# Kernel tuning notes

Measured on AMD Instinct MI355X. Metric: run time of the kernel, lower is better.

## Reference

```python
import jax, jax.numpy as jnp
import numpy as np

NUM_PITCHES = 88
H_FEAT = 188
LSTM_UNITS = 48
N_STATES = 5
CTX_HID = 16
CTX_OUT = 4


def _glorot(key, shape):
    fan_in, fan_out = shape[1], shape[0]
    lim = (6.0 / (fan_in + fan_out)) ** 0.5
    return jax.random.uniform(key, shape, jnp.float32, -lim, lim)


def setup_inputs() -> dict:
    key = jax.random.key(0)
    ks = jax.random.split(key, 16)
    B, T = 16, 256
    pitch_features = jax.random.normal(ks[0], (B, NUM_PITCHES, H_FEAT, T), jnp.float32)
    prev_context = jax.random.uniform(ks[1], (B, NUM_PITCHES, 3), jnp.float32)
    # context net params
    fc1_w = _glorot(ks[2], (CTX_HID, 3)); fc1_b = jnp.zeros((CTX_HID,), jnp.float32)
    fc2_w = _glorot(ks[3], (CTX_HID, CTX_HID)); fc2_b = jnp.zeros((CTX_HID,), jnp.float32)
    fc3_w = _glorot(ks[4], (CTX_OUT, CTX_HID)); fc3_b = jnp.zeros((CTX_OUT,), jnp.float32)
    # lstm1: input H_FEAT+4 -> 48; gates order i,f,g,o (torch convention)
    in1 = H_FEAT + CTX_OUT
    lstm1_wih = _glorot(ks[5], (4 * LSTM_UNITS, in1))
    lstm1_whh = _glorot(ks[6], (4 * LSTM_UNITS, LSTM_UNITS))
    lstm1_bih = jnp.zeros((4 * LSTM_UNITS,), jnp.float32)
    lstm1_bhh = jnp.zeros((4 * LSTM_UNITS,), jnp.float32)
    lstm2_wih = _glorot(ks[7], (4 * LSTM_UNITS, LSTM_UNITS))
    lstm2_whh = _glorot(ks[8], (4 * LSTM_UNITS, LSTM_UNITS))
    lstm2_bih = jnp.zeros((4 * LSTM_UNITS,), jnp.float32)
    lstm2_bhh = jnp.zeros((4 * LSTM_UNITS,), jnp.float32)
    fc_states_w = _glorot(ks[9], (N_STATES, LSTM_UNITS))
    fc_states_b = jnp.zeros((N_STATES,), jnp.float32)
    return dict(pitch_features=pitch_features, prev_context=prev_context,
                fc1_w=fc1_w, fc1_b=fc1_b, fc2_w=fc2_w, fc2_b=fc2_b,
                fc3_w=fc3_w, fc3_b=fc3_b,
                lstm1_wih=lstm1_wih, lstm1_whh=lstm1_whh, lstm1_bih=lstm1_bih, lstm1_bhh=lstm1_bhh,
                lstm2_wih=lstm2_wih, lstm2_whh=lstm2_whh, lstm2_bih=lstm2_bih, lstm2_bhh=lstm2_bhh,
                fc_states_w=fc_states_w, fc_states_b=fc_states_b)


def _lstm_scan(x, wih, whh, bih, bhh):
    # x: (S, N, In); zero init state; returns (S, N, U)
    S, N, _ = x.shape
    U = whh.shape[1]
    xg = jnp.einsum('sni,gi->sng', x, wih) + bih + bhh  # precompute input gates

    def step(carry, xg_t):
        h, c = carry
        g = xg_t + h @ whh.T  # (N, 4U)
        i, f, gg, o = jnp.split(g, 4, axis=-1)
        c = jax.nn.sigmoid(f) * c + jax.nn.sigmoid(i) * jnp.tanh(gg)
        h = jax.nn.sigmoid(o) * jnp.tanh(c)
        return (h, c), h

    init = (jnp.zeros((N, U), x.dtype), jnp.zeros((N, U), x.dtype))
    _, hs = jax.lax.scan(step, init, xg)
    return hs


def reference(pitch_features, prev_context,
              fc1_w, fc1_b, fc2_w, fc2_b, fc3_w, fc3_b,
              lstm1_wih, lstm1_whh, lstm1_bih, lstm1_bhh,
              lstm2_wih, lstm2_whh, lstm2_bih, lstm2_bhh,
              fc_states_w, fc_states_b):
    B, P, H, T = pitch_features.shape
    # Context net (context never updates across t in the original loop)
    x = jax.nn.relu(prev_context @ fc1_w.T + fc1_b)
    x = jax.nn.relu(x @ fc2_w.T + fc2_b)
    ctx_emb = x @ fc3_w.T + fc3_b  # (B, P, 4)
    # Each timestep t is independent: LSTM runs over the pitch axis (len 88)
    # with zero initial state every step. Fold (B, T) into batch N.
    pf = jnp.transpose(pitch_features, (1, 0, 3, 2)).reshape(P, B * T, H)  # (P, BT, H)
    ce = jnp.broadcast_to(ctx_emb[:, None, :, :], (B, T, P, CTX_OUT))
    ce = jnp.transpose(ce, (2, 0, 1, 3)).reshape(P, B * T, CTX_OUT)
    seq = jnp.concatenate([pf, ce], axis=-1)  # (P, BT, H+4)
    h = _lstm_scan(seq, lstm1_wih, lstm1_whh, lstm1_bih, lstm1_bhh)
    h = _lstm_scan(h, lstm2_wih, lstm2_whh, lstm2_bih, lstm2_bhh)
    logits = h @ fc_states_w.T + fc_states_b  # (P, BT, 5)
    logits = logits.reshape(P, B, T, N_STATES)
    logits = jnp.transpose(logits, (1, 0, 3, 2))  # (B, P, 5, T)
    return jax.nn.softmax(logits, axis=2)
```

## Files before the change

kernel.cpp:

```cpp
#include <hip/hip_runtime.h>
#include <hip/hip_bf16.h>
#include <cstdint>

#define P_ 88
#define B_ 16
#define T_ 256
#define H_ 188
#define G_ 192
#define U_ 48
#define N_ 4096

typedef __attribute__((ext_vector_type(8))) short bf16x8;
typedef __attribute__((ext_vector_type(8))) _Float16 f16x8;
typedef __attribute__((ext_vector_type(4))) float f32x4;

__device__ __forceinline__ float sigf(float x) {
  return __builtin_amdgcn_rcpf(1.0f + __expf(-x));
}
__device__ __forceinline__ float tanh_f(float x) {
  return 1.0f - 2.0f * __builtin_amdgcn_rcpf(1.0f + __expf(2.0f * x));
}
__device__ __forceinline__ float hs2f(unsigned short s) {
  union { unsigned short u; _Float16 h; } x;
  x.u = s;
  return (float)x.h;
}
__device__ __forceinline__ unsigned short f2hs(float v) {
  union { _Float16 h; unsigned short s; } x;
  x.h = (_Float16)v;
  return x.s;
}

__device__ __forceinline__ void lds_barrier() {
  asm volatile("s_waitcnt lgkmcnt(0)\n\ts_barrier" ::: "memory");
}

__global__ void ctx_kernel(const float* __restrict__ pc,
                           const float* __restrict__ fc1w, const float* __restrict__ fc1b,
                           const float* __restrict__ fc2w, const float* __restrict__ fc2b,
                           const float* __restrict__ fc3w, const float* __restrict__ fc3b,
                           const float* __restrict__ wih1,
                           const float* __restrict__ bih1, const float* __restrict__ bhh1,
                           float* __restrict__ ctxg) {
  int bp = blockIdx.x * 64 + threadIdx.x;
  if (bp >= B_ * P_) return;
  float p0 = pc[bp * 3 + 0], p1 = pc[bp * 3 + 1], p2 = pc[bp * 3 + 2];
  float x1[16], x2[16];
#pragma unroll
  for (int jj = 0; jj < 16; ++jj)
    x1[jj] = fmaxf(0.f, fc1w[jj * 3 + 0] * p0 + fc1w[jj * 3 + 1] * p1 + fc1w[jj * 3 + 2] * p2 + fc1b[jj]);
#pragma unroll
  for (int jj = 0; jj < 16; ++jj) {
    float s = fc2b[jj];
#pragma unroll
    for (int i = 0; i < 16; ++i) s += fc2w[jj * 16 + i] * x1[i];
    x2[jj] = fmaxf(0.f, s);
  }
  float ce[4];
#pragma unroll
  for (int jj = 0; jj < 4; ++jj) {
    float s = fc3b[jj];
#pragma unroll
    for (int i = 0; i < 16; ++i) s += fc3w[jj * 16 + i] * x2[i];
    ce[jj] = s;
  }
  float* op = ctxg + (size_t)bp * G_;
  for (int g = 0; g < G_; ++g) {
    const float* wr = wih1 + (size_t)g * G_ + H_;
    op[g] = bih1[g] + bhh1[g] + ce[0] * wr[0] + ce[1] * wr[1] + ce[2] * wr[2] + ce[3] * wr[3];
  }
}

__global__ __launch_bounds__(256) void wfrag_kernel(const float* __restrict__ wih1,
                                                    f16x8* __restrict__ wfrag) {
  const int idx = blockIdx.x * 256 + threadIdx.x;
  if (idx >= 12 * 6 * 64) return;
  const int l = idx & 63;
  const int kc = (idx >> 6) % 6;
  const int j = idx / 384;
  const int g = j * 16 + (l & 15);
  const int k0 = kc * 32 + (l >> 4) * 8;
  f16x8 v;
#pragma unroll
  for (int e = 0; e < 8; ++e) {
    const int k = k0 + e;
    const float wv = (k < H_) ? wih1[(size_t)g * G_ + k] : 0.f;
    v[e] = (_Float16)wv;
  }
  wfrag[idx] = v;
}

__global__ __launch_bounds__(256, 3) void gemm_mfma(const float* __restrict__ pf,
                                                    const f16x8* __restrict__ wfrag,
                                                    const float* __restrict__ ctxg,
                                                    unsigned short* __restrict__ xg2) {
  const int bp = blockIdx.x >> 1, tb = blockIdx.x & 1;
  const int p = bp % P_, b = bp / P_;
  const int tid = threadIdx.x;
  const int w = tid >> 6, l = tid & 63;
  const int lj = l & 15, lq = l >> 4;

  __shared__ __align__(16) char ldsraw[49152];
  _Float16(*Ahi)[34] = (_Float16(*)[34])ldsraw;
  _Float16(*Alo)[34] = (_Float16(*)[34])(ldsraw + 8704);

  float cg[12];
#pragma unroll
  for (int jn = 0; jn < 12; ++jn)
    cg[jn] = ctxg[(size_t)bp * G_ + jn * 16 + lj];

  f32x4 acc[2][12];
#pragma unroll
  for (int mt = 0; mt < 2; ++mt)
#pragma unroll
    for (int jn = 0; jn < 12; ++jn)
#pragma unroll
      for (int r = 0; r < 4; ++r) acc[mt][jn][r] = 0.f;

  const float* Ab = pf + (size_t)bp * H_ * T_ + tb * 128;
  const int kl = tid >> 5;
  const int t4 = (tid & 31) * 4;

  for (int kc = 0; kc < 6; ++kc) {
    __syncthreads();
#pragma unroll
    for (int rr = 0; rr < 4; ++rr) {
      const int kk = rr * 8 + kl;
      const int kg = kc * 32 + kk;
      float a0 = 0.f, a1 = 0.f, a2 = 0.f, a3 = 0.f;
      if (kg < H_) {
        const float4 v = *(const float4*)(Ab + (size_t)kg * T_ + t4);
        a0 = v.x; a1 = v.y; a2 = v.z; a3 = v.w;
      }
      const _Float16 h0 = (_Float16)a0, h1 = (_Float16)a1;
      const _Float16 h2 = (_Float16)a2, h3 = (_Float16)a3;
      Ahi[t4 + 0][kk] = h0; Alo[t4 + 0][kk] = (_Float16)(a0 - (float)h0);
      Ahi[t4 + 1][kk] = h1; Alo[t4 + 1][kk] = (_Float16)(a1 - (float)h1);
      Ahi[t4 + 2][kk] = h2; Alo[t4 + 2][kk] = (_Float16)(a2 - (float)h2);
      Ahi[t4 + 3][kk] = h3; Alo[t4 + 3][kk] = (_Float16)(a3 - (float)h3);
    }
    __syncthreads();
    const int trow = w * 32;
    const f16x8 ahi0 = *(const f16x8*)&Ahi[trow + lj][lq * 8];
    const f16x8 ahi1 = *(const f16x8*)&Ahi[trow + 16 + lj][lq * 8];
    const f16x8 alo0 = *(const f16x8*)&Alo[trow + lj][lq * 8];
    const f16x8 alo1 = *(const f16x8*)&Alo[trow + 16 + lj][lq * 8];
#pragma unroll
    for (int jn = 0; jn < 12; ++jn) {
      const f16x8 wf = wfrag[(jn * 6 + kc) * 64 + l];
      acc[0][jn] = __builtin_amdgcn_mfma_f32_16x16x32_f16(ahi0, wf, acc[0][jn], 0, 0, 0);
      acc[1][jn] = __builtin_amdgcn_mfma_f32_16x16x32_f16(ahi1, wf, acc[1][jn], 0, 0, 0);
      acc[0][jn] = __builtin_amdgcn_mfma_f32_16x16x32_f16(alo0, wf, acc[0][jn], 0, 0, 0);
      acc[1][jn] = __builtin_amdgcn_mfma_f32_16x16x32_f16(alo1, wf, acc[1][jn], 0, 0, 0);
    }
  }
  __syncthreads();

  unsigned short* Cst = (unsigned short*)ldsraw + w * 6144;
#pragma unroll
  for (int mt = 0; mt < 2; ++mt)
#pragma unroll
    for (int jn = 0; jn < 12; ++jn)
#pragma unroll
      for (int r = 0; r < 4; ++r)
        Cst[mt * 3072 + jn * 256 + r * 64 + l] = f2hs(acc[mt][jn][r] + cg[jn]);
  const int nb0 = b * 16 + tb * 8 + w * 2;
  unsigned short* gb = xg2 + ((size_t)p * 256 + nb0) * 3072;
#pragma unroll
  for (int rr = 0; rr < 12; ++rr) {
    const uint4 v = *(const uint4*)(Cst + rr * 512 + l * 8);
    *(uint4*)(gb + rr * 512 + l * 8) = v;
  }
}

__global__ __launch_bounds__(256, 2) void scan_mfma(
    const unsigned short* __restrict__ xg2,
    const float* __restrict__ whh1, const float* __restrict__ wih2,
    const float* __restrict__ whh2, const float* __restrict__ bih2,
    const float* __restrict__ bhh2, const float* __restrict__ fcw,
    const float* __restrict__ fcb, float* __restrict__ out) {
  __shared__ __align__(16) _Float16 h12[16][104];
  __shared__ __align__(16) float gs1[8][196];
  __shared__ __align__(16) float gs2[8][196];
  __shared__ __align__(16) float h2f[8][52];
  __shared__ __align__(16) float fcws[5 * 48];
  __shared__ float logit_s[5][8];
  __shared__ float prob_s[5][8];

  const int tid = threadIdx.x;
  const int w = tid >> 6;
  const int l = tid & 63;
  const int lj = l & 15;
  const int lq = l >> 4;
  const int grp = blockIdx.x >> 1;
  const int half = blockIdx.x & 1;
  const int n0 = blockIdx.x * 8;
  const int b = n0 >> 8, t0 = n0 & 255;

  f16x8 b1[3][2];
  f16x8 b2f[3][3];
  float bias2r[3];
#pragma unroll
  for (int i = 0; i < 3; ++i) {
    const int j = w * 48 + i * 16 + lj;
    bias2r[i] = bih2[j] + bhh2[j];
#pragma unroll
    for (int kc = 0; kc < 2; ++kc)
#pragma unroll
      for (int e = 0; e < 8; ++e) {
        const int u = kc * 32 + lq * 8 + e;
        b1[i][kc][e] = (u < U_) ? (_Float16)whh1[j * U_ + u] : (_Float16)0.f;
      }
#pragma unroll
    for (int kc = 0; kc < 3; ++kc)
#pragma unroll
      for (int e = 0; e < 8; ++e) {
        const int k = kc * 32 + lq * 8 + e;
        b2f[i][kc][e] = (k < U_) ? (_Float16)wih2[j * U_ + k]
                                 : (_Float16)whh2[j * U_ + (k - U_)];
      }
  }

  for (int e = tid; e < 16 * 104 / 2; e += 256) ((unsigned int*)h12)[e] = 0u;
  for (int e = tid; e < 5 * U_; e += 256) fcws[e] = fcw[e];

  const int tn0 = tid / U_, tu0 = tid % U_;
  const int tn1 = (256 + tid) / U_, tu1 = (256 + tid) % U_;
  const bool has2 = (tid < 128);
  float c1s[2] = {0.f, 0.f}, c2s[2] = {0.f, 0.f};

  const bool fcth = tid < 40;
  const int fk = tid >> 3, fn = tid & 7;
  const float fcbr = fcth ? fcb[fk] : 0.f;
  const bool stth = tid >= 96 && tid < 136;
  const int sk = (tid - 96) >> 3, sn = (tid - 96) & 7;
  const bool smth = tid >= 192 && tid < 200;
  const int smn = tid - 192;

  unsigned short xp[12];
  {
    const size_t pb = (size_t)grp * 3072;
#pragma unroll
    for (int i = 0; i < 3; ++i)
#pragma unroll
      for (int r = 0; r < 4; ++r)
        xp[i * 4 + r] = (lq < 2)
            ? xg2[pb + (size_t)((w * 3 + i) * 256 + r * 64 + (half * 2 + lq) * 16 + lj)]
            : (unsigned short)0;
  }
  lds_barrier();

  for (int p = -1; p < P_; ++p) {
    const _Float16* hr = &h12[lj][0];
    const f16x8 f0 = *(const f16x8*)(hr + lq * 8);
    const f16x8 f1 = *(const f16x8*)(hr + 32 + lq * 8);
    const f16x8 f2 = *(const f16x8*)(hr + 64 + lq * 8);
    if (p >= 0) {
      f32x4 dH[3];
#pragma unroll
      for (int i = 0; i < 3; ++i) {
        dH[i][0] = bias2r[i]; dH[i][1] = bias2r[i];
        dH[i][2] = bias2r[i]; dH[i][3] = bias2r[i];
      }
#pragma unroll
      for (int i = 0; i < 3; ++i)
        dH[i] = __builtin_amdgcn_mfma_f32_16x16x32_f16(f0, b2f[i][0], dH[i], 0, 0, 0);
#pragma unroll
      for (int i = 0; i < 3; ++i)
        dH[i] = __builtin_amdgcn_mfma_f32_16x16x32_f16(f1, b2f[i][1], dH[i], 0, 0, 0);
#pragma unroll
      for (int i = 0; i < 3; ++i)
        dH[i] = __builtin_amdgcn_mfma_f32_16x16x32_f16(f2, b2f[i][2], dH[i], 0, 0, 0);
      if (lq < 2) {
#pragma unroll
        for (int i = 0; i < 3; ++i)
#pragma unroll
          for (int r = 0; r < 4; ++r)
            gs2[lq * 4 + r][w * 48 + i * 16 + lj] = dH[i][r];
      }
    }
    if (p >= 1 && fcth) {
      float a = fcbr;
#pragma unroll
      for (int uq = 0; uq < 12; ++uq) {
        f32x4 hv = *(const f32x4*)&h2f[fn][uq * 4];
        f32x4 wv = *(const f32x4*)&fcws[fk * 48 + uq * 4];
        a += hv[0] * wv[0] + hv[1] * wv[1] + hv[2] * wv[2] + hv[3] * wv[3];
      }
      logit_s[fk][fn] = a;
    }
    if (p >= 2 && stth) {
      out[(((size_t)b * P_ + (p - 2)) * 5 + sk) * T_ + t0 + sn] = prob_s[sk][sn];
    }
    __builtin_amdgcn_sched_barrier(0);
    if (p < P_ - 1) {
      f32x4 cH[3];
#pragma unroll
      for (int i = 0; i < 3; ++i)
#pragma unroll
        for (int r = 0; r < 4; ++r) cH[i][r] = hs2f(xp[i * 4 + r]);
      if (p < P_ - 2) {
        const size_t pb = (size_t)((p + 2) * 256 + grp) * 3072;
#pragma unroll
        for (int i = 0; i < 3; ++i)
#pragma unroll
          for (int r = 0; r < 4; ++r)
            xp[i * 4 + r] = (lq < 2)
                ? xg2[pb + (size_t)((w * 3 + i) * 256 + r * 64 + (half * 2 + lq) * 16 + lj)]
                : (unsigned short)0;
      }
#pragma unroll
      for (int i = 0; i < 3; ++i)
        cH[i] = __builtin_amdgcn_mfma_f32_16x16x32_f16(f0, b1[i][0], cH[i], 0, 0, 0);
#pragma unroll
      for (int i = 0; i < 3; ++i)
        cH[i] = __builtin_amdgcn_mfma_f32_16x16x32_f16(f1, b1[i][1], cH[i], 0, 0, 0);
      if (lq < 2) {
#pragma unroll
        for (int i = 0; i < 3; ++i)
#pragma unroll
          for (int r = 0; r < 4; ++r)
            gs1[lq * 4 + r][w * 48 + i * 16 + lj] = cH[i][r];
      }
    }
    lds_barrier();
    if (p >= 0) {
      {
        const int n = tn0, u = tu0;
        const float ig = gs2[n][u], fg = gs2[n][48 + u];
        const float gg = gs2[n][96 + u], og = gs2[n][144 + u];
        const float cc = sigf(fg) * c2s[0] + sigf(ig) * tanh_f(gg);
        c2s[0] = cc;
        const float h = sigf(og) * tanh_f(cc);
        h12[n][48 + u] = (_Float16)h;
        h2f[n][u] = h;
      }
      if (has2) {
        const int n = tn1, u = tu1;
        const float ig = gs2[n][u], fg = gs2[n][48 + u];
        const float gg = gs2[n][96 + u], og = gs2[n][144 + u];
        const float cc = sigf(fg) * c2s[1] + sigf(ig) * tanh_f(gg);
        c2s[1] = cc;
        const float h = sigf(og) * tanh_f(cc);
        h12[n][48 + u] = (_Float16)h;
        h2f[n][u] = h;
      }
    }
    if (p < P_ - 1) {
      {
        const int n = tn0, u = tu0;
        const float ig = gs1[n][u], fg = gs1[n][48 + u];
        const float gg = gs1[n][96 + u], og = gs1[n][144 + u];
        const float cc = sigf(fg) * c1s[0] + sigf(ig) * tanh_f(gg);
        c1s[0] = cc;
        h12[n][u] = (_Float16)(sigf(og) * tanh_f(cc));
      }
      if (has2) {
        const int n = tn1, u = tu1;
        const float ig = gs1[n][u], fg = gs1[n][48 + u];
        const float gg = gs1[n][96 + u], og = gs1[n][144 + u];
        const float cc = sigf(fg) * c1s[1] + sigf(ig) * tanh_f(gg);
        c1s[1] = cc;
        h12[n][u] = (_Float16)(sigf(og) * tanh_f(cc));
      }
    }
    if (p >= 1 && smth) {
      const int n = smn;
      const float l0 = logit_s[0][n], l1 = logit_s[1][n], l2 = logit_s[2][n],
                  l3 = logit_s[3][n], l4 = logit_s[4][n];
      const float m = fmaxf(fmaxf(fmaxf(l0, l1), fmaxf(l2, l3)), l4);
      const float e0 = __expf(l0 - m), e1 = __expf(l1 - m), e2 = __expf(l2 - m),
                  e3 = __expf(l3 - m), e4 = __expf(l4 - m);
      const float rs = __builtin_amdgcn_rcpf(e0 + e1 + e2 + e3 + e4);
      prob_s[0][n] = e0 * rs; prob_s[1][n] = e1 * rs; prob_s[2][n] = e2 * rs;
      prob_s[3][n] = e3 * rs; prob_s[4][n] = e4 * rs;
    }
    lds_barrier();
  }
  if (fcth) {
    float a = fcbr;
#pragma unroll
    for (int uq = 0; uq < 12; ++uq) {
      f32x4 hv = *(const f32x4*)&h2f[fn][uq * 4];
      f32x4 wv = *(const f32x4*)&fcws[fk * 48 + uq * 4];
      a += hv[0] * wv[0] + hv[1] * wv[1] + hv[2] * wv[2] + hv[3] * wv[3];
    }
    logit_s[fk][fn] = a;
  }
  if (stth) {
    out[(((size_t)b * P_ + (P_ - 2)) * 5 + sk) * T_ + t0 + sn] = prob_s[sk][sn];
  }
  lds_barrier();
  if (smth) {
    const int n = smn;
    const float l0 = logit_s[0][n], l1 = logit_s[1][n], l2 = logit_s[2][n],
                l3 = logit_s[3][n], l4 = logit_s[4][n];
    const float m = fmaxf(fmaxf(fmaxf(l0, l1), fmaxf(l2, l3)), l4);
    const float e0 = __expf(l0 - m), e1 = __expf(l1 - m), e2 = __expf(l2 - m),
                e3 = __expf(l3 - m), e4 = __expf(l4 - m);
    const float rs = __builtin_amdgcn_rcpf(e0 + e1 + e2 + e3 + e4);
    prob_s[0][n] = e0 * rs; prob_s[1][n] = e1 * rs; prob_s[2][n] = e2 * rs;
    prob_s[3][n] = e3 * rs; prob_s[4][n] = e4 * rs;
  }
  lds_barrier();
  if (stth) {
    out[(((size_t)b * P_ + (P_ - 1)) * 5 + sk) * T_ + t0 + sn] = prob_s[sk][sn];
  }
}

extern "C" void kernel_launch(void* const* d_in, const int* in_sizes, int n_in,
                              void* d_out, int out_size, void* d_ws, size_t ws_size,
                              hipStream_t stream) {
  const float* pf   = (const float*)d_in[0];
  const float* pc   = (const float*)d_in[1];
  const float* fc1w = (const float*)d_in[2];
  const float* fc1b = (const float*)d_in[3];
  const float* fc2w = (const float*)d_in[4];
  const float* fc2b = (const float*)d_in[5];
  const float* fc3w = (const float*)d_in[6];
  const float* fc3b = (const float*)d_in[7];
  const float* wih1 = (const float*)d_in[8];
  const float* whh1 = (const float*)d_in[9];
  const float* bih1 = (const float*)d_in[10];
  const float* bhh1 = (const float*)d_in[11];
  const float* wih2 = (const float*)d_in[12];
  const float* whh2 = (const float*)d_in[13];
  const float* bih2 = (const float*)d_in[14];
  const float* bhh2 = (const float*)d_in[15];
  const float* fcw  = (const float*)d_in[16];
  const float* fcb  = (const float*)d_in[17];
  float* out = (float*)d_out;

  char* wsp = (char*)d_ws;
  float* ctxg = (float*)wsp;
  const size_t CTXG_BYTES = (size_t)B_ * P_ * G_ * sizeof(float);
  f16x8* wfrag = (f16x8*)(wsp + CTXG_BYTES);
  const size_t WFRAG_BYTES = (size_t)12 * 6 * 64 * 16;
  unsigned short* xg2 = (unsigned short*)(wsp + CTXG_BYTES + WFRAG_BYTES);

  ctx_kernel<<<22, 64, 0, stream>>>(pc, fc1w, fc1b, fc2w, fc2b, fc3w, fc3b,
                                    wih1, bih1, bhh1, ctxg);
  wfrag_kernel<<<18, 256, 0, stream>>>(wih1, wfrag);
  gemm_mfma<<<B_ * P_ * 2, 256, 0, stream>>>(pf, wfrag, ctxg, xg2);
  scan_mfma<<<N_ / 8, 256, 0, stream>>>(xg2, whh1, wih2, whh2,
                                        bih2, bhh2, fcw, fcb, out);
}
```

Before: 397.2 us.

## Permute gate columns so LSTM cell update runs in MFMA registers via lane shuffles

Reorders the gate columns of the layer-1 input projection and of the layer-2 weights so each 16-column MFMA tile holds all four gates for a set of units. The cell update can then be done directly on the MFMA accumulators using xor-lane shuffles, instead of scattering gates to shared memory and reading them back after a barrier. The hidden-state buffer becomes double-buffered, which lets the layer-2 and layer-1 steps each finish within their own phase. The FC, store and softmax work is spread across waves. The goal is to cut LDS round trips and per-step barrier work on the serial recurrence, at the cost of shuffle overhead and more complex index mapping.

```diff
diff --git a/kernel.cpp b/kernel.cpp
--- a/kernel.cpp
+++ b/kernel.cpp
@@ -33,6 +33,28 @@
 
 __device__ __forceinline__ void lds_barrier() {
   asm volatile("s_waitcnt lgkmcnt(0)\n\ts_barrier" ::: "memory");
+}
+
+__device__ __forceinline__ void qtrans(const f32x4 v, int l,
+                                       float& g0, float& g1, float& g2, float& g3) {
+  const bool qo = (l & 1);
+  const float e0 = __shfl_xor((float)v[1], 1);
+  const float e1 = __shfl_xor((float)v[0], 1);
+  const float e2 = __shfl_xor((float)v[3], 1);
+  const float e3 = __shfl_xor((float)v[2], 1);
+  const float a0 = qo ? e0 : v[0];
+  const float a1 = qo ? v[1] : e1;
+  const float a2 = qo ? e2 : v[2];
+  const float a3 = qo ? v[3] : e3;
+  const bool q2 = (l & 2);
+  const float f0 = __shfl_xor(a2, 2);
+  const float f1 = __shfl_xor(a3, 2);
+  const float f2 = __shfl_xor(a0, 2);
+  const float f3 = __shfl_xor(a1, 2);
+  g0 = q2 ? f0 : a0;
+  g1 = q2 ? f1 : a1;
+  g2 = q2 ? a2 : f2;
+  g3 = q2 ? a3 : f3;
 }
 
 __global__ void ctx_kernel(const float* __restrict__ pc,
@@ -160,10 +182,18 @@
 #pragma unroll
   for (int mt = 0; mt < 2; ++mt)
 #pragma unroll
-    for (int jn = 0; jn < 12; ++jn)
+    for (int jn = 0; jn < 12; ++jn) {
+      const int g = jn * 16 + lj;
+      const int t = g / 48;
+      const int rem = g - 48 * t;
+      const int sw = rem / 12;
+      const int ul = rem - 12 * sw;
+      const int c = ul * 4 + t;
+      const int slot = (sw * 3 + (c >> 4)) * 256 + lq * 16 + (c & 15);
 #pragma unroll
       for (int r = 0; r < 4; ++r)
-        Cst[mt * 3072 + jn * 256 + r * 64 + l] = f2hs(acc[mt][jn][r] + cg[jn]);
+        Cst[mt * 3072 + slot + r * 64] = f2hs(acc[mt][jn][r] + cg[jn]);
+    }
   const int nb0 = b * 16 + tb * 8 + w * 2;
   unsigned short* gb = xg2 + ((size_t)p * 256 + nb0) * 3072;
 #pragma unroll
@@ -179,21 +209,16 @@
     const float* __restrict__ whh2, const float* __restrict__ bih2,
     const float* __restrict__ bhh2, const float* __restrict__ fcw,
     const float* __restrict__ fcb, float* __restrict__ out) {
-  __shared__ __align__(16) _Float16 h12[16][104];
-  __shared__ __align__(16) float gs1[8][196];
-  __shared__ __align__(16) float gs2[8][196];
-  __shared__ __align__(16) float h2f[8][52];
+  __shared__ __align__(16) _Float16 hbuf[2][16][120];
+  __shared__ __align__(16) float h2f[2][8][52];
   __shared__ __align__(16) float fcws[5 * 48];
   __shared__ float logit_s[5][8];
   __shared__ float prob_s[5][8];
 
   const int tid = threadIdx.x;
-  const int w = tid >> 6;
-  const int l = tid & 63;
-  const int lj = l & 15;
-  const int lq = l >> 4;
-  const int grp = blockIdx.x >> 1;
-  const int half = blockIdx.x & 1;
+  const int w = tid >> 6, l = tid & 63;
+  const int lj = l & 15, lq = l >> 4;
+  const int grp = blockIdx.x >> 1, half = blockIdx.x & 1;
   const int n0 = blockIdx.x * 8;
   const int b = n0 >> 8, t0 = n0 & 255;
 
@@ -202,7 +227,9 @@
   float bias2r[3];
 #pragma unroll
   for (int i = 0; i < 3; ++i) {
-    const int j = w * 48 + i * 16 + lj;
+    const int c = i * 16 + lj;
+    const int ul = c >> 2, t = c & 3;
+    const int j = t * 48 + w * 12 + ul;
     bias2r[i] = bih2[j] + bhh2[j];
 #pragma unroll
     for (int kc = 0; kc < 2; ++kc)
@@ -221,21 +248,23 @@
       }
   }
 
-  for (int e = tid; e < 16 * 104 / 2; e += 256) ((unsigned int*)h12)[e] = 0u;
+  for (int e = tid; e < 2 * 16 * 120 / 2; e += 256) ((unsigned int*)hbuf)[e] = 0u;
+  for (int e = tid; e < 2 * 8 * 52; e += 256) ((float*)h2f)[e] = 0.f;
   for (int e = tid; e < 5 * U_; e += 256) fcws[e] = fcw[e];
 
-  const int tn0 = tid / U_, tu0 = tid % U_;
-  const int tn1 = (256 + tid) / U_, tu1 = (256 + tid) % U_;
-  const bool has2 = (tid < 128);
-  float c1s[2] = {0.f, 0.f}, c2s[2] = {0.f, 0.f};
-
-  const bool fcth = tid < 40;
-  const int fk = tid >> 3, fn = tid & 7;
+  const int qn = lq * 4 + (l & 3);
+  const int kk = (l >> 2) & 3;
+  float c1s[3] = {0.f, 0.f, 0.f}, c2s[3] = {0.f, 0.f, 0.f};
+
+  const bool fcth = (l >= 32 && l < 42);
+  const int fi = w * 10 + (l - 32);
+  const int fk = (fi >> 3) < 5 ? (fi >> 3) : 0, fn = fi & 7;
   const float fcbr = fcth ? fcb[fk] : 0.f;
-  const bool stth = tid >= 96 && tid < 136;
-  const int sk = (tid - 96) >> 3, sn = (tid - 96) & 7;
-  const bool smth = tid >= 192 && tid < 200;
-  const int smn = tid - 192;
+  const bool stth = (l >= 42 && l < 52);
+  const int ts = w * 10 + (l - 42);
+  const int sk = (ts >> 3) < 5 ? (ts >> 3) : 0, sn = ts & 7;
+  const bool smth = (l >= 52 && l < 54);
+  const int smn = w * 2 + (l - 52);
 
   unsigned short xp[12];
   {
@@ -251,11 +280,13 @@
   lds_barrier();
 
   for (int p = -1; p < P_; ++p) {
-    const _Float16* hr = &h12[lj][0];
-    const f16x8 f0 = *(const f16x8*)(hr + lq * 8);
-    const f16x8 f1 = *(const f16x8*)(hr + 32 + lq * 8);
-    const f16x8 f2 = *(const f16x8*)(hr + 64 + lq * 8);
+    const int cur = p & 1, alt = cur ^ 1;
     if (p >= 0) {
+      const _Float16* hc = &hbuf[cur][lj][0];
+      const _Float16* ha = &hbuf[alt][lj][0];
+      const f16x8 f0 = *(const f16x8*)(hc + lq * 8);
+      const f16x8 f1 = *(const f16x8*)(((lq < 2) ? hc : ha) + 32 + lq * 8);
+      const f16x8 f2 = *(const f16x8*)(ha + 64 + lq * 8);
       f32x4 dH[3];
 #pragma unroll
       for (int i = 0; i < 3; ++i) {
@@ -271,29 +302,36 @@
 #pragma unroll
       for (int i = 0; i < 3; ++i)
         dH[i] = __builtin_amdgcn_mfma_f32_16x16x32_f16(f2, b2f[i][2], dH[i], 0, 0, 0);
-      if (lq < 2) {
-#pragma unroll
-        for (int i = 0; i < 3; ++i)
-#pragma unroll
-          for (int r = 0; r < 4; ++r)
-            gs2[lq * 4 + r][w * 48 + i * 16 + lj] = dH[i][r];
-      }
-    }
-    if (p >= 1 && fcth) {
-      float a = fcbr;
-#pragma unroll
-      for (int uq = 0; uq < 12; ++uq) {
-        f32x4 hv = *(const f32x4*)&h2f[fn][uq * 4];
-        f32x4 wv = *(const f32x4*)&fcws[fk * 48 + uq * 4];
-        a += hv[0] * wv[0] + hv[1] * wv[1] + hv[2] * wv[2] + hv[3] * wv[3];
-      }
-      logit_s[fk][fn] = a;
-    }
-    if (p >= 2 && stth) {
-      out[(((size_t)b * P_ + (p - 2)) * 5 + sk) * T_ + t0 + sn] = prob_s[sk][sn];
-    }
-    __builtin_amdgcn_sched_barrier(0);
+      if (l < 32) {
+#pragma unroll
+        for (int i = 0; i < 3; ++i) {
+          float g0, g1, g2, g3;
+          qtrans(dH[i], l, g0, g1, g2, g3);
+          const float cc = sigf(g1) * c2s[i] + sigf(g0) * tanh_f(g2);
+          c2s[i] = cc;
+          const float h = sigf(g3) * tanh_f(cc);
+          const int u = w * 12 + i * 4 + kk;
+          hbuf[cur][qn][48 + u] = (_Float16)h;
+          h2f[cur][qn][u] = h;
+        }
+      } else if (fcth && p >= 1) {
+        float a = fcbr;
+#pragma unroll
+        for (int uq = 0; uq < 12; ++uq) {
+          f32x4 hv = *(const f32x4*)&h2f[alt][fn][uq * 4];
+          f32x4 wv = *(const f32x4*)&fcws[fk * 48 + uq * 4];
+          a += hv[0] * wv[0] + hv[1] * wv[1] + hv[2] * wv[2] + hv[3] * wv[3];
+        }
+        logit_s[fk][fn] = a;
+      } else if (stth && p >= 2) {
+        out[(((size_t)b * P_ + (p - 2)) * 5 + sk) * T_ + t0 + sn] = prob_s[sk][sn];
+      }
+    }
+    lds_barrier();
     if (p < P_ - 1) {
+      const _Float16* hc = &hbuf[cur][lj][0];
+      const f16x8 f0 = *(const f16x8*)(hc + lq * 8);
+      const f16x8 f1 = *(const f16x8*)(hc + 32 + lq * 8);
       f32x4 cH[3];
 #pragma unroll
       for (int i = 0; i < 3; ++i)
@@ -315,56 +353,19 @@
 #pragma unroll
       for (int i = 0; i < 3; ++i)
         cH[i] = __builtin_amdgcn_mfma_f32_16x16x32_f16(f1, b1[i][1], cH[i], 0, 0, 0);
-      if (lq < 2) {
-#pragma unroll
-        for (int i = 0; i < 3; ++i)
-#pragma unroll
-          for (int r = 0; r < 4; ++r)
-            gs1[lq * 4 + r][w * 48 + i * 16 + lj] = cH[i][r];
-      }
-    }
-    lds_barrier();
-    if (p >= 0) {
-      {
-        const int n = tn0, u = tu0;
-        const float ig = gs2[n][u], fg = gs2[n][48 + u];
-        const float gg = gs2[n][96 + u], og = gs2[n][144 + u];
-        const float cc = sigf(fg) * c2s[0] + sigf(ig) * tanh_f(gg);
-        c2s[0] = cc;
-        const float h = sigf(og) * tanh_f(cc);
-        h12[n][48 + u] = (_Float16)h;
-        h2f[n][u] = h;
-      }
-      if (has2) {
-        const int n = tn1, u = tu1;
-        const float ig = gs2[n][u], fg = gs2[n][48 + u];
-        const float gg = gs2[n][96 + u], og = gs2[n][144 + u];
-        const float cc = sigf(fg) * c2s[1] + sigf(ig) * tanh_f(gg);
-        c2s[1] = cc;
-        const float h = sigf(og) * tanh_f(cc);
-        h12[n][48 + u] = (_Float16)h;
-        h2f[n][u] = h;
-      }
-    }
-    if (p < P_ - 1) {
-      {
-        const int n = tn0, u = tu0;
-        const float ig = gs1[n][u], fg = gs1[n][48 + u];
-        const float gg = gs1[n][96 + u], og = gs1[n][144 + u];
-        const float cc = sigf(fg) * c1s[0] + sigf(ig) * tanh_f(gg);
-        c1s[0] = cc;
-        h12[n][u] = (_Float16)(sigf(og) * tanh_f(cc));
-      }
-      if (has2) {
-        const int n = tn1, u = tu1;
-        const float ig = gs1[n][u], fg = gs1[n][48 + u];
-        const float gg = gs1[n][96 + u], og = gs1[n][144 + u];
-        const float cc = sigf(fg) * c1s[1] + sigf(ig) * tanh_f(gg);
-        c1s[1] = cc;
-        h12[n][u] = (_Float16)(sigf(og) * tanh_f(cc));
-      }
-    }
-    if (p >= 1 && smth) {
+      if (l < 32) {
+#pragma unroll
+        for (int i = 0; i < 3; ++i) {
+          float g0, g1, g2, g3;
+          qtrans(cH[i], l, g0, g1, g2, g3);
+          const float cc = sigf(g1) * c1s[i] + sigf(g0) * tanh_f(g2);
+          c1s[i] = cc;
+          const int u = w * 12 + i * 4 + kk;
+          hbuf[alt][qn][u] = (_Float16)(sigf(g3) * tanh_f(cc));
+        }
+      }
+    }
+    if (smth && p >= 1) {
       const int n = smn;
       const float l0 = logit_s[0][n], l1 = logit_s[1][n], l2 = logit_s[2][n],
                   l3 = logit_s[3][n], l4 = logit_s[4][n];
@@ -377,11 +378,12 @@
     }
     lds_barrier();
   }
+  const int parL = (P_ - 1) & 1;
   if (fcth) {
     float a = fcbr;
 #pragma unroll
     for (int uq = 0; uq < 12; ++uq) {
-      f32x4 hv = *(const f32x4*)&h2f[fn][uq * 4];
+      f32x4 hv = *(const f32x4*)&h2f[parL][fn][uq * 4];
       f32x4 wv = *(const f32x4*)&fcws[fk * 48 + uq * 4];
       a += hv[0] * wv[0] + hv[1] * wv[1] + hv[2] * wv[2] + hv[3] * wv[3];
     }
```

After: 487.7 us. +22.8%, slower.

## Fuse LSTM1 input-projection GEMM into the recurrent scan kernel with double-buffered staging

Applied to the files above, without the earlier changes.

Removes the separate wfrag and gemm_mfma kernels and the fp16 xg2 intermediate buffer. The scan kernel now holds W_ih1 fragments in registers and computes each pitch's input gates itself with MFMA on hi/lo split fp16 features. The features for the next pitch are prefetched into double-buffered LDS while the current step runs. This avoids writing and re-reading the large gate tensor through global memory. In exchange the serial scan loop gets 36 extra MFMAs per step plus heavier register pressure, which may lower occupancy.

```diff
diff --git a/kernel.cpp b/kernel.cpp
--- a/kernel.cpp
+++ b/kernel.cpp
@@ -10,7 +10,6 @@
 #define U_ 48
 #define N_ 4096
 
-typedef __attribute__((ext_vector_type(8))) short bf16x8;
 typedef __attribute__((ext_vector_type(8))) _Float16 f16x8;
 typedef __attribute__((ext_vector_type(4))) float f32x4;
 
@@ -19,16 +18,6 @@
 }
 __device__ __forceinline__ float tanh_f(float x) {
   return 1.0f - 2.0f * __builtin_amdgcn_rcpf(1.0f + __expf(2.0f * x));
-}
-__device__ __forceinline__ float hs2f(unsigned short s) {
-  union { unsigned short u; _Float16 h; } x;
-  x.u = s;
-  return (float)x.h;
-}
-__device__ __forceinline__ unsigned short f2hs(float v) {
-  union { _Float16 h; unsigned short s; } x;
-  x.h = (_Float16)v;
-  return x.s;
 }
 
 __device__ __forceinline__ void lds_barrier() {
@@ -71,114 +60,13 @@
   }
 }
 
-__global__ __launch_bounds__(256) void wfrag_kernel(const float* __restrict__ wih1,
-                                                    f16x8* __restrict__ wfrag) {
-  const int idx = blockIdx.x * 256 + threadIdx.x;
-  if (idx >= 12 * 6 * 64) return;
-  const int l = idx & 63;
-  const int kc = (idx >> 6) % 6;
-  const int j = idx / 384;
-  const int g = j * 16 + (l & 15);
-  const int k0 = kc * 32 + (l >> 4) * 8;
-  f16x8 v;
-#pragma unroll
-  for (int e = 0; e < 8; ++e) {
-    const int k = k0 + e;
-    const float wv = (k < H_) ? wih1[(size_t)g * G_ + k] : 0.f;
-    v[e] = (_Float16)wv;
-  }
-  wfrag[idx] = v;
-}
-
-__global__ __launch_bounds__(256, 3) void gemm_mfma(const float* __restrict__ pf,
-                                                    const f16x8* __restrict__ wfrag,
-                                                    const float* __restrict__ ctxg,
-                                                    unsigned short* __restrict__ xg2) {
-  const int bp = blockIdx.x >> 1, tb = blockIdx.x & 1;
-  const int p = bp % P_, b = bp / P_;
-  const int tid = threadIdx.x;
-  const int w = tid >> 6, l = tid & 63;
-  const int lj = l & 15, lq = l >> 4;
-
-  __shared__ __align__(16) char ldsraw[49152];
-  _Float16(*Ahi)[34] = (_Float16(*)[34])ldsraw;
-  _Float16(*Alo)[34] = (_Float16(*)[34])(ldsraw + 8704);
-
-  float cg[12];
-#pragma unroll
-  for (int jn = 0; jn < 12; ++jn)
-    cg[jn] = ctxg[(size_t)bp * G_ + jn * 16 + lj];
-
-  f32x4 acc[2][12];
-#pragma unroll
-  for (int mt = 0; mt < 2; ++mt)
-#pragma unroll
-    for (int jn = 0; jn < 12; ++jn)
-#pragma unroll
-      for (int r = 0; r < 4; ++r) acc[mt][jn][r] = 0.f;
-
-  const float* Ab = pf + (size_t)bp * H_ * T_ + tb * 128;
-  const int kl = tid >> 5;
-  const int t4 = (tid & 31) * 4;
-
-  for (int kc = 0; kc < 6; ++kc) {
-    __syncthreads();
-#pragma unroll
-    for (int rr = 0; rr < 4; ++rr) {
-      const int kk = rr * 8 + kl;
-      const int kg = kc * 32 + kk;
-      float a0 = 0.f, a1 = 0.f, a2 = 0.f, a3 = 0.f;
-      if (kg < H_) {
-        const float4 v = *(const float4*)(Ab + (size_t)kg * T_ + t4);
-        a0 = v.x; a1 = v.y; a2 = v.z; a3 = v.w;
-      }
-      const _Float16 h0 = (_Float16)a0, h1 = (_Float16)a1;
-      const _Float16 h2 = (_Float16)a2, h3 = (_Float16)a3;
-      Ahi[t4 + 0][kk] = h0; Alo[t4 + 0][kk] = (_Float16)(a0 - (float)h0);
-      Ahi[t4 + 1][kk] = h1; Alo[t4 + 1][kk] = (_Float16)(a1 - (float)h1);
-      Ahi[t4 + 2][kk] = h2; Alo[t4 + 2][kk] = (_Float16)(a2 - (float)h2);
-      Ahi[t4 + 3][kk] = h3; Alo[t4 + 3][kk] = (_Float16)(a3 - (float)h3);
-    }
-    __syncthreads();
-    const int trow = w * 32;
-    const f16x8 ahi0 = *(const f16x8*)&Ahi[trow + lj][lq * 8];
-    const f16x8 ahi1 = *(const f16x8*)&Ahi[trow + 16 + lj][lq * 8];
-    const f16x8 alo0 = *(const f16x8*)&Alo[trow + lj][lq * 8];
-    const f16x8 alo1 = *(const f16x8*)&Alo[trow + 16 + lj][lq * 8];
-#pragma unroll
-    for (int jn = 0; jn < 12; ++jn) {
-      const f16x8 wf = wfrag[(jn * 6 + kc) * 64 + l];
-      acc[0][jn] = __builtin_amdgcn_mfma_f32_16x16x32_f16(ahi0, wf, acc[0][jn], 0, 0, 0);
-      acc[1][jn] = __builtin_amdgcn_mfma_f32_16x16x32_f16(ahi1, wf, acc[1][jn], 0, 0, 0);
-      acc[0][jn] = __builtin_amdgcn_mfma_f32_16x16x32_f16(alo0, wf, acc[0][jn], 0, 0, 0);
-      acc[1][jn] = __builtin_amdgcn_mfma_f32_16x16x32_f16(alo1, wf, acc[1][jn], 0, 0, 0);
-    }
-  }
-  __syncthreads();
-
-  unsigned short* Cst = (unsigned short*)ldsraw + w * 6144;
-#pragma unroll
-  for (int mt = 0; mt < 2; ++mt)
-#pragma unroll
-    for (int jn = 0; jn < 12; ++jn)
-#pragma unroll
-      for (int r = 0; r < 4; ++r)
-        Cst[mt * 3072 + jn * 256 + r * 64 + l] = f2hs(acc[mt][jn][r] + cg[jn]);
-  const int nb0 = b * 16 + tb * 8 + w * 2;
-  unsigned short* gb = xg2 + ((size_t)p * 256 + nb0) * 3072;
-#pragma unroll
-  for (int rr = 0; rr < 12; ++rr) {
-    const uint4 v = *(const uint4*)(Cst + rr * 512 + l * 8);
-    *(uint4*)(gb + rr * 512 + l * 8) = v;
-  }
-}
-
-__global__ __launch_bounds__(256, 2) void scan_mfma(
-    const unsigned short* __restrict__ xg2,
-    const float* __restrict__ whh1, const float* __restrict__ wih2,
-    const float* __restrict__ whh2, const float* __restrict__ bih2,
-    const float* __restrict__ bhh2, const float* __restrict__ fcw,
-    const float* __restrict__ fcb, float* __restrict__ out) {
+__global__ __launch_bounds__(256, 2) void scan_fused(
+    const float* __restrict__ pf, const float* __restrict__ ctxg,
+    const float* __restrict__ wih1, const float* __restrict__ whh1,
+    const float* __restrict__ wih2, const float* __restrict__ whh2,
+    const float* __restrict__ bih2, const float* __restrict__ bhh2,
+    const float* __restrict__ fcw, const float* __restrict__ fcb,
+    float* __restrict__ out) {
   __shared__ __align__(16) _Float16 h12[16][104];
   __shared__ __align__(16) float gs1[8][196];
   __shared__ __align__(16) float gs2[8][196];
@@ -186,19 +74,18 @@
   __shared__ __align__(16) float fcws[5 * 48];
   __shared__ float logit_s[5][8];
   __shared__ float prob_s[5][8];
+  __shared__ __align__(16) _Float16 pfhi[2][8][200];
+  __shared__ __align__(16) _Float16 pflo[2][8][200];
 
   const int tid = threadIdx.x;
-  const int w = tid >> 6;
-  const int l = tid & 63;
-  const int lj = l & 15;
-  const int lq = l >> 4;
-  const int grp = blockIdx.x >> 1;
-  const int half = blockIdx.x & 1;
+  const int w = tid >> 6, l = tid & 63;
+  const int lj = l & 15, lq = l >> 4;
   const int n0 = blockIdx.x * 8;
   const int b = n0 >> 8, t0 = n0 & 255;
 
   f16x8 b1[3][2];
   f16x8 b2f[3][3];
+  f16x8 wf[3][6];
   float bias2r[3];
 #pragma unroll
   for (int i = 0; i < 3; ++i) {
@@ -219,10 +106,22 @@
         b2f[i][kc][e] = (k < U_) ? (_Float16)wih2[j * U_ + k]
                                  : (_Float16)whh2[j * U_ + (k - U_)];
       }
-  }
-
-  for (int e = tid; e < 16 * 104 / 2; e += 256) ((unsigned int*)h12)[e] = 0u;
+#pragma unroll
+    for (int kc = 0; kc < 6; ++kc)
+#pragma unroll
+      for (int e = 0; e < 8; ++e) {
+        const int k = kc * 32 + lq * 8 + e;
+        wf[i][kc][e] = (k < H_) ? (_Float16)wih1[(size_t)j * G_ + k] : (_Float16)0.f;
+      }
+  }
+
+  for (int e = tid; e < 16 * 104 / 2; e += 256) ((unsigned*)h12)[e] = 0u;
+  for (int e = tid; e < 1600; e += 256) {
+    ((unsigned*)pfhi)[e] = 0u;
+    ((unsigned*)pflo)[e] = 0u;
+  }
   for (int e = tid; e < 5 * U_; e += 256) fcws[e] = fcw[e];
+  lds_barrier();
 
   const int tn0 = tid / U_, tu0 = tid % U_;
   const int tn1 = (256 + tid) / U_, tu1 = (256 + tid) % U_;
@@ -237,25 +136,70 @@
   const bool smth = tid >= 192 && tid < 200;
   const int smn = tid - 192;
 
-  unsigned short xp[12];
-  {
-    const size_t pb = (size_t)grp * 3072;
-#pragma unroll
-    for (int i = 0; i < 3; ++i)
-#pragma unroll
-      for (int r = 0; r < 4; ++r)
-        xp[i * 4 + r] = (lq < 2)
-            ? xg2[pb + (size_t)((w * 3 + i) * 256 + r * 64 + (half * 2 + lq) * 16 + lj)]
-            : (unsigned short)0;
-  }
-  lds_barrier();
+  const int sh = tid >> 3, stl = tid & 7;
+  const float* pfb = pf + (size_t)b * P_ * H_ * T_ + (size_t)sh * T_ + t0 + stl;
+
+#pragma unroll
+  for (int it = 0; it < 6; ++it) {
+    const int h = sh + it * 32;
+    if (h < H_) {
+      const float v0 = pfb[(size_t)it * 32 * T_];
+      const float v1 = pfb[(size_t)H_ * T_ + (size_t)it * 32 * T_];
+      const _Float16 h0 = (_Float16)v0, h1 = (_Float16)v1;
+      pfhi[0][stl][h] = h0; pflo[0][stl][h] = (_Float16)(v0 - (float)h0);
+      pfhi[1][stl][h] = h1; pflo[1][stl][h] = (_Float16)(v1 - (float)h1);
+    }
+  }
+  lds_barrier();
+
+  const float* cgbase = ctxg + (size_t)b * P_ * G_ + w * 48 + lj;
+  float cgN[3];
+  f32x4 xgC[3];
+#pragma unroll
+  for (int i = 0; i < 3; ++i) {
+    const float c0 = cgbase[i * 16];
+    xgC[i][0] = c0; xgC[i][1] = c0; xgC[i][2] = c0; xgC[i][3] = c0;
+    cgN[i] = cgbase[G_ + i * 16];
+  }
+  const float* cgp = cgbase + 2 * G_;
+
+#define INGEMM(ACC, RB)                                                        \
+  {                                                                            \
+    _Pragma("unroll") for (int c = 0; c < 6; ++c) {                            \
+      const f16x8 ah = *(const f16x8*)&pfhi[RB][lj & 7][c * 32 + lq * 8];      \
+      const f16x8 al = *(const f16x8*)&pflo[RB][lj & 7][c * 32 + lq * 8];      \
+      ACC[0] = __builtin_amdgcn_mfma_f32_16x16x32_f16(ah, wf[0][c], ACC[0], 0, 0, 0); \
+      ACC[1] = __builtin_amdgcn_mfma_f32_16x16x32_f16(ah, wf[1][c], ACC[1], 0, 0, 0); \
+      ACC[2] = __builtin_amdgcn_mfma_f32_16x16x32_f16(ah, wf[2][c], ACC[2], 0, 0, 0); \
+      ACC[0] = __builtin_amdgcn_mfma_f32_16x16x32_f16(al, wf[0][c], ACC[0], 0, 0, 0); \
+      ACC[1] = __builtin_amdgcn_mfma_f32_16x16x32_f16(al, wf[1][c], ACC[1], 0, 0, 0); \
+      ACC[2] = __builtin_amdgcn_mfma_f32_16x16x32_f16(al, wf[2][c], ACC[2], 0, 0, 0); \
+    }                                                                          \
+  }
+
+  INGEMM(xgC, 0);
+  lds_barrier();
+
+  const float* pfstage = pfb + (size_t)2 * H_ * T_;
 
   for (int p = -1; p < P_; ++p) {
+    const bool doL2 = (p >= 0), doL1 = (p < P_ - 1);
+    const bool doProd = (p <= 85), doStage = (p <= 84);
+    const int prb = p & 1;
+    const int pwb = prb ^ 1;
+
+    float pv[6];
+    if (doStage) {
+#pragma unroll
+      for (int it = 0; it < 6; ++it)
+        pv[it] = (sh + it * 32 < H_) ? pfstage[(size_t)it * 32 * T_] : 0.f;
+    }
+
     const _Float16* hr = &h12[lj][0];
     const f16x8 f0 = *(const f16x8*)(hr + lq * 8);
     const f16x8 f1 = *(const f16x8*)(hr + 32 + lq * 8);
-    const f16x8 f2 = *(const f16x8*)(hr + 64 + lq * 8);
-    if (p >= 0) {
+    if (doL2) {
+      const f16x8 f2 = *(const f16x8*)(hr + 64 + lq * 8);
       f32x4 dH[3];
 #pragma unroll
       for (int i = 0; i < 3; ++i) {
@@ -279,7 +223,7 @@
             gs2[lq * 4 + r][w * 48 + i * 16 + lj] = dH[i][r];
       }
     }
-    if (p >= 1 && fcth) {
+    if (fcth && p >= 1) {
       float a = fcbr;
 #pragma unroll
       for (int uq = 0; uq < 12; ++uq) {
@@ -289,29 +233,15 @@
       }
       logit_s[fk][fn] = a;
     }
-    if (p >= 2 && stth) {
+    if (stth && p >= 2) {
       out[(((size_t)b * P_ + (p - 2)) * 5 + sk) * T_ + t0 + sn] = prob_s[sk][sn];
     }
     __builtin_amdgcn_sched_barrier(0);
-    if (p < P_ - 1) {
+    if (doL1) {
       f32x4 cH[3];
 #pragma unroll
       for (int i = 0; i < 3; ++i)
-#pragma unroll
-        for (int r = 0; r < 4; ++r) cH[i][r] = hs2f(xp[i * 4 + r]);
-      if (p < P_ - 2) {
-        const size_t pb = (size_t)((p + 2) * 256 + grp) * 3072;
-#pragma unroll
-        for (int i = 0; i < 3; ++i)
-#pragma unroll
-          for (int r = 0; r < 4; ++r)
-            xp[i * 4 + r] = (lq < 2)
-                ? xg2[pb + (size_t)((w * 3 + i) * 256 + r * 64 + (half * 2 + lq) * 16 + lj)]
-                : (unsigned short)0;
-      }
-#pragma unroll
-      for (int i = 0; i < 3; ++i)
-        cH[i] = __builtin_amdgcn_mfma_f32_16x16x32_f16(f0, b1[i][0], cH[i], 0, 0, 0);
+        cH[i] = __builtin_amdgcn_mfma_f32_16x16x32_f16(f0, b1[i][0], xgC[i], 0, 0, 0);
 #pragma unroll
       for (int i = 0; i < 3; ++i)
         cH[i] = __builtin_amdgcn_mfma_f32_16x16x32_f16(f1, b1[i][1], cH[i], 0, 0, 0);
@@ -323,8 +253,36 @@
             gs1[lq * 4 + r][w * 48 + i * 16 + lj] = cH[i][r];
       }
     }
+    if (doProd) {
+      f32x4 xgP[3];
+#pragma unroll
+      for (int i = 0; i < 3; ++i) {
+        xgP[i][0] = cgN[i]; xgP[i][1] = cgN[i];
+        xgP[i][2] = cgN[i]; xgP[i][3] = cgN[i];
+      }
+      INGEMM(xgP, prb);
+      if (doStage) {
+#pragma unroll
+        for (int i = 0; i < 3; ++i) cgN[i] = cgp[i * 16];
+        cgp += G_;
+      }
+#pragma unroll
+      for (int i = 0; i < 3; ++i) xgC[i] = xgP[i];
+    }
+    if (doStage) {
+#pragma unroll
+      for (int it = 0; it < 6; ++it) {
+        const int h = sh + it * 32;
+        if (h < H_) {
+          const _Float16 hi = (_Float16)pv[it];
+          pfhi[pwb][stl][h] = hi;
+          pflo[pwb][stl][h] = (_Float16)(pv[it] - (float)hi);
+        }
+      }
+      pfstage += (size_t)H_ * T_;
+    }
     lds_barrier();
-    if (p >= 0) {
+    if (doL2) {
       {
         const int n = tn0, u = tu0;
         const float ig = gs2[n][u], fg = gs2[n][48 + u];
@@ -346,7 +304,7 @@
         h2f[n][u] = h;
       }
     }
-    if (p < P_ - 1) {
+    if (doL1) {
       {
         const int n = tn0, u = tu0;
         const float ig = gs1[n][u], fg = gs1[n][48 + u];
@@ -364,7 +322,7 @@
         h12[n][u] = (_Float16)(sigf(og) * tanh_f(cc));
       }
     }
-    if (p >= 1 && smth) {
+    if (smth && p >= 1) {
       const int n = smn;
       const float l0 = logit_s[0][n], l1 = logit_s[1][n], l2 = logit_s[2][n],
                   l3 = logit_s[3][n], l4 = logit_s[4][n];
@@ -431,17 +389,10 @@
   const float* fcb  = (const float*)d_in[17];
   float* out = (float*)d_out;
 
-  char* wsp = (char*)d_ws;
-  float* ctxg = (float*)wsp;
-  const size_t CTXG_BYTES = (size_t)B_ * P_ * G_ * sizeof(float);
-  f16x8* wfrag = (f16x8*)(wsp + CTXG_BYTES);
-  const size_t WFRAG_BYTES = (size_t)12 * 6 * 64 * 16;
-  unsigned short* xg2 = (unsigned short*)(wsp + CTXG_BYTES + WFRAG_BYTES);
+  float* ctxg = (float*)d_ws;
 
   ctx_kernel<<<22, 64, 0, stream>>>(pc, fc1w, fc1b, fc2w, fc2b, fc3w, fc3b,
                                     wih1, bih1, bhh1, ctxg);
-  wfrag_kernel<<<18, 256, 0, stream>>>(wih1, wfrag);
-  gemm_mfma<<<B_ * P_ * 2, 256, 0, stream>>>(pf, wfrag, ctxg, xg2);
-  scan_mfma<<<N_ / 8, 256, 0, stream>>>(xg2, whh1, wih2, whh2,
-                                        bih2, bhh2, fcw, fcb, out);
-}
+  scan_fused<<<N_ / 8, 256, 0, stream>>>(pf, ctxg, wih1, whh1, wih2, whh2,
+                                         bih2, bhh2, fcw, fcb, out);
+}
```

After: 432.0 us. 1.09x slower.
